# Kernel tuning notes

Hardware: AMD Instinct MI355X
Metric: run time of the kernel (lower is better)

Reference implementation:

```python
import jax, jax.numpy as jnp
import numpy as np

NEG = -1e30  # stand-in for -inf that keeps logaddexp grad-safe


def _ctc_neg_log_likelihood(predictions, labels):
    # predictions: [B, T, C] logits; labels: [B, L] int, -1 = padding.
    # tf.nn.ctc_loss(blank_index=-1) => blank class is C-1.
    B, T, C = predictions.shape
    L = labels.shape[1]
    S = 2 * L + 1
    blank = C - 1

    label_len = jnp.sum((labels != -1).astype(jnp.int32), axis=-1)  # [B]
    labels_c = jnp.where(labels < 0, 0, labels).astype(jnp.int32)

    # Extended label sequence: blank, l1, blank, l2, ..., blank  -> [B, S]
    ext = jnp.full((B, S), blank, dtype=jnp.int32)
    ext = ext.at[:, 1::2].set(labels_c)

    # s-2 transition allowed only at label positions (odd s) with ext[s] != ext[s-2]
    same = jnp.concatenate([jnp.zeros((B, 2), bool), ext[:, 2:] == ext[:, :-2]], axis=1)
    is_label_pos = (jnp.arange(S) % 2 == 1)[None, :]
    allow2 = is_label_pos & ~same  # [B, S]

    # valid extended positions per example: s < 2*label_len + 1
    valid = jnp.arange(S)[None, :] < (2 * label_len + 1)[:, None]  # [B, S]

    log_probs = jax.nn.log_softmax(predictions, axis=-1)  # [B, T, C]
    # emission log-prob for each extended-label slot: [B, T, S]
    lp_ext = jnp.take_along_axis(log_probs, jnp.broadcast_to(ext[:, None, :], (B, T, S)), axis=2)

    has_lab = label_len > 0
    alpha0 = jnp.full((B, S), NEG, dtype=log_probs.dtype)
    alpha0 = alpha0.at[:, 0].set(lp_ext[:, 0, 0])
    alpha0 = alpha0.at[:, 1].set(jnp.where(has_lab, lp_ext[:, 0, 1], NEG))
    alpha0 = jnp.where(valid, alpha0, NEG)

    def step(alpha, lp_t):
        a1 = alpha
        a2 = jnp.pad(alpha, ((0, 0), (1, 0)), constant_values=NEG)[:, :S]
        a3 = jnp.pad(alpha, ((0, 0), (2, 0)), constant_values=NEG)[:, :S]
        a3 = jnp.where(allow2, a3, NEG)
        new = jnp.logaddexp(jnp.logaddexp(a1, a2), a3) + lp_t
        new = jnp.where(valid, new, NEG)
        return new, None

    lp_rest = jnp.moveaxis(lp_ext[:, 1:], 1, 0)  # [T-1, B, S]
    alphaT, _ = jax.lax.scan(step, alpha0, lp_rest)

    idx1 = (2 * label_len)[:, None]              # final blank
    idx2 = jnp.maximum(idx1 - 1, 0)              # final label
    a_end1 = jnp.take_along_axis(alphaT, idx1, axis=1)[:, 0]
    a_end2 = jnp.take_along_axis(alphaT, idx2, axis=1)[:, 0]
    a_end2 = jnp.where(has_lab, a_end2, NEG)
    log_lik = jnp.logaddexp(a_end1, a_end2)
    return -log_lik  # [B]


def setup_inputs() -> dict:
    key = jax.random.key(0)
    k1, k2 = jax.random.split(key)
    B, T, C, L = 1024, 384, 96, 48
    labels = jax.random.randint(k1, (B, L), 0, C - 1).astype(jnp.int64)
    predictions = jax.random.normal(k2, (B, T, C), dtype=jnp.float32)
    return {"labels": labels, "predictions": predictions}


def reference(labels, predictions):
    per_example = _ctc_neg_log_likelihood(predictions, labels)
    return jnp.mean(per_example)
```

## Files before the change

kernel.cpp:

```cpp
#include <hip/hip_runtime.h>

constexpr int Tt = 384;
constexpr int Cc = 96;
constexpr int Ll = 48;
constexpr int Gg = 8;
constexpr int NG = 24;

#define L2E 1.4426950408889634f
#define LN2 0.6931471805599453f
#define LNEG (-3.0e38f)

template <int CTRL, int RM = 0xF>
__device__ __forceinline__ float dppf(float x) {
    return __int_as_float(
        __builtin_amdgcn_update_dpp(0, __float_as_int(x), CTRL, RM, 0xF, true));
}
template <int CTRL>
__device__ __forceinline__ int dppi(int x) {
    return __builtin_amdgcn_update_dpp(0, x, CTRL, 0xF, 0xF, true);
}
__device__ __forceinline__ float bcast63(float x) {
    return __int_as_float(__builtin_amdgcn_readlane(__float_as_int(x), 63));
}
__device__ __forceinline__ float wsum(float x) {
    x += dppf<0x111>(x);
    x += dppf<0x112>(x);
    x += dppf<0x114>(x);
    x += dppf<0x118>(x);
    x += dppf<0x142, 0xA>(x);
    x += dppf<0x143, 0xC>(x);
    return bcast63(x);
}
__device__ __forceinline__ float shup1(float x) { return dppf<0x138>(x); }
__device__ __forceinline__ float shdn1(float x) { return dppf<0x130>(x); }
__device__ __forceinline__ float exp2i(int d) {
    d = d < -126 ? -126 : (d > 126 ? 126 : d);
    return __int_as_float((d + 127) << 23);
}

__global__ __launch_bounds__(512) void ctc_zsum(const float* __restrict__ pred,
                                                float* __restrict__ zs,
                                                float* __restrict__ out) {
    const int b    = blockIdx.x;
    const int lane = threadIdx.x & 63;
    const int wv   = threadIdx.x >> 6;
    const float2* rp2 = (const float2*)(pred + (size_t)b * Tt * Cc);
    __shared__ double part[8];

    if (b == 0 && threadIdx.x == 0) out[0] = 0.0f;

    const int t0 = wv * 48;
    double acc = 0.0;
    float2 qa = (lane < 48) ? rp2[(size_t)t0 * 48 + lane] : make_float2(-1e4f, -1e4f);
    for (int j = 0; j < 48; ++j) {
        float2 qn = qa;
        if (j + 1 < 48)
            qn = (lane < 48) ? rp2[(size_t)(t0 + j + 1) * 48 + lane]
                             : make_float2(-1e4f, -1e4f);
        float ex = __builtin_amdgcn_exp2f(qa.x * L2E);
        float ey = __builtin_amdgcn_exp2f(qa.y * L2E);
        float z  = wsum(ex + ey);
        acc += (double)__log2f(z);
        qa = qn;
    }
    if (lane == 0) part[wv] = acc;
    __syncthreads();
    if (threadIdx.x == 0) {
        double s = 0.0;
#pragma unroll
        for (int w = 0; w < 8; ++w) s += part[w];
        zs[b] = (float)s;
    }
}


template <bool FWD>
__device__ __forceinline__ void dp_load(const float* __restrict__ rp, float* ql,
                                        float* qb, int g, int labv) {
#pragma unroll
    for (int j = 0; j < Gg; ++j) {
        int k = g * Gg + j;
        int t = FWD ? k : (Tt - 1 - k);
        ql[j] = rp[t * Cc + labv];
        qb[j] = rp[t * Cc + 95];
    }
}

template <bool FWD>
__device__ __forceinline__ void dp_group(const float* ql, const float* qb,
                                         float allow2f, float& st_e, float& st_o,
                                         int& ls, float& f, float& a2f) {
    float el[Gg], eb[Gg];
#pragma unroll
    for (int j = 0; j < Gg; ++j) {
        el[j] = __builtin_amdgcn_exp2f(ql[j] * L2E);
        eb[j] = __builtin_amdgcn_exp2f(qb[j] * L2E);
    }
#pragma unroll
    for (int j = 0; j < Gg; ++j) {
        if (FWD) {
            float sh = shup1(st_o);
            float t0 = st_e + st_o;
            float ne = fmaf(f, sh, st_e) * eb[j];
            float no = fmaf(a2f, sh, t0) * el[j];
            st_e = ne; st_o = no;
        } else {
            float en = shdn1(st_e);
            float on = shdn1(st_o);
            float ne = (st_e + st_o) * eb[j];
            float no = fmaf(a2f, on, fmaf(f, en, st_o)) * el[j];
            st_e = ne; st_o = no;
        }
    }
    float m = fmaxf(st_e, st_o);
    bool z  = (m == 0.0f);
    int eb2 = (__float_as_int(m) >> 23) & 0xFF;
    eb2 = eb2 > 253 ? 253 : eb2;
    float r = z ? 1.0f : __int_as_float((254 - eb2) << 23);
    st_e *= r; st_o *= r;
    ls += z ? 0 : (eb2 - 127);
#pragma unroll
    for (int it = 0; it < 8; ++it) {
        int lsn = FWD ? dppi<0x138>(ls) : dppi<0x130>(ls);
        ls = z ? lsn : ls;
    }
    int lsn2 = FWD ? dppi<0x138>(ls) : dppi<0x130>(ls);
    f   = exp2i(lsn2 - ls);
    a2f = allow2f * f;
}

template <bool FWD>
__device__ __forceinline__ void run_half(const float* __restrict__ rp, int labv,
                                         float allow2f, float& st_e, float& st_o,
                                         int& ls, float& f, float& a2f) {
    float qlA[Gg], qbA[Gg], qlB[Gg], qbB[Gg], qlC[Gg], qbC[Gg], qlD[Gg], qbD[Gg];
    dp_load<FWD>(rp, qlA, qbA, 0, labv);
    dp_load<FWD>(rp, qlB, qbB, 1, labv);
    dp_load<FWD>(rp, qlC, qbC, 2, labv);
    dp_load<FWD>(rp, qlD, qbD, 3, labv);
    for (int g4 = 0; g4 < 5; ++g4) {
        int gb = g4 * 4;
        dp_group<FWD>(qlA, qbA, allow2f, st_e, st_o, ls, f, a2f);
        dp_load<FWD>(rp, qlA, qbA, gb + 4, labv);
        dp_group<FWD>(qlB, qbB, allow2f, st_e, st_o, ls, f, a2f);
        dp_load<FWD>(rp, qlB, qbB, gb + 5, labv);
        dp_group<FWD>(qlC, qbC, allow2f, st_e, st_o, ls, f, a2f);
        dp_load<FWD>(rp, qlC, qbC, gb + 6, labv);
        dp_group<FWD>(qlD, qbD, allow2f, st_e, st_o, ls, f, a2f);
        dp_load<FWD>(rp, qlD, qbD, gb + 7, labv);
    }
    dp_group<FWD>(qlA, qbA, allow2f, st_e, st_o, ls, f, a2f);
    dp_group<FWD>(qlB, qbB, allow2f, st_e, st_o, ls, f, a2f);
    dp_group<FWD>(qlC, qbC, allow2f, st_e, st_o, ls, f, a2f);
    dp_group<FWD>(qlD, qbD, allow2f, st_e, st_o, ls, f, a2f);
}

__global__ __launch_bounds__(128) void ctc_dp(const int* __restrict__ labels,
                                              const float* __restrict__ pred,
                                              const float* __restrict__ zs,
                                              float* __restrict__ out,
                                              float invB) {
    const int b    = blockIdx.x;
    const int lane = threadIdx.x & 63;
    const int wv   = threadIdx.x >> 6;
    const float* rp = pred + (size_t)b * Tt * Cc;

    __shared__ float sbe[64], sbo[64];
    __shared__ int   slsb[64];

    float zsb = zs[b];

    int v = (lane < Ll) ? labels[(size_t)b * Ll + lane] : -1;
    int present = (lane < Ll) && (v != -1);
    int labv = (v < 0) ? 0 : v;
    unsigned long long pm = __ballot(present);
    int len = __popcll(pm);
    int lab_p = __shfl(labv, (lane - 1) & 63, 64);
    int lab_n = __shfl(labv, (lane + 1) & 63, 64);

    float st_e, st_o = 0.0f, f = 1.0f, a2f, allow2f;
    int   ls = 0;

    if (wv == 0) {
        allow2f = (lane >= 1 && labv != lab_p) ? 1.0f : 0.0f;
        st_e = (lane == 0) ? 1.0f : 0.0f;
        a2f = allow2f;
        run_half<true>(rp, labv, allow2f, st_e, st_o, ls, f, a2f);
    } else {
        allow2f = (labv != lab_n) ? 1.0f : 0.0f;
        st_e = (lane == len) ? 1.0f : 0.0f;
        a2f = allow2f;
        run_half<false>(rp, labv, allow2f, st_e, st_o, ls, f, a2f);
        sbe[lane]  = st_e;
        sbo[lane]  = st_o;
        slsb[lane] = ls;
    }
    __syncthreads();

    if (wv == 0) {
        float sh  = shup1(st_o);
        int   lsu = dppi<0x138>(ls);
        float fup = exp2i(lsu - ls);
        float Ae = fmaf(fup, sh, st_e);
        float Ao = fmaf(allow2f * fup, sh, st_e + st_o);
        float be = sbe[lane], bo = sbo[lane];
        float base = (float)(ls + slsb[lane]);
        float l1 = (Ae > 0.0f && be > 0.0f) ? __log2f(Ae) + __log2f(be) + base : LNEG;
        float l2 = (Ao > 0.0f && bo > 0.0f) ? __log2f(Ao) + __log2f(bo) + base : LNEG;
        float mm = fmaxf(l1, l2);
#pragma unroll
        for (int off = 32; off >= 1; off >>= 1) mm = fmaxf(mm, __shfl_xor(mm, off, 64));
        float ss = exp2f(l1 - mm) + exp2f(l2 - mm);
#pragma unroll
        for (int off = 32; off >= 1; off >>= 1) ss += __shfl_xor(ss, off, 64);
        if (lane == 0) {
            float ll = (mm + __log2f(ss) - zsb) * LN2;
            atomicAdd(out, -ll * invB);
        }
    }
}

extern "C" void kernel_launch(void* const* d_in, const int* in_sizes, int n_in,
                              void* d_out, int out_size, void* d_ws, size_t ws_size,
                              hipStream_t stream) {
    const int*   labels = (const int*)d_in[0];
    const float* pred   = (const float*)d_in[1];
    float*       out    = (float*)d_out;
    float*       zs     = (float*)d_ws;

    const int B = in_sizes[0] / Ll;

    hipLaunchKernelGGL(ctc_zsum, dim3(B), dim3(512), 0, stream, pred, zs, out);
    hipLaunchKernelGGL(ctc_dp, dim3(B), dim3(128), 0, stream,
                       labels, pred, zs, out, 1.0f / (float)B);
}
```

Baseline: 248.8 us.

## Fuse softmax normalizer and forward-backward DP into one kernel with deterministic mean

The separate log-sum-exp kernel is merged into the DP kernel. Two waves run the forward and backward recursions while six more waves in the same 512-thread block compute the per-row normalizer over 64 timesteps each. The atomic mean is replaced by a per-example NLL buffer and a small reduction kernel. Register prefetch depth drops from four groups to two, presumably to allow launch_bounds(512,8) occupancy. The aim is to remove a launch and the re-read of predictions, and to overlap the normalizer work with the latency-bound DP, at the cost of shallower load prefetching and a hard-coded B=1024 in the mean kernel.

Result: faster. 237.3 us (-4.6%).

```diff
diff --git a/kernel.cpp b/kernel.cpp
--- a/kernel.cpp
+++ b/kernel.cpp
@@ -37,42 +37,6 @@
     d = d < -126 ? -126 : (d > 126 ? 126 : d);
     return __int_as_float((d + 127) << 23);
 }
-
-__global__ __launch_bounds__(512) void ctc_zsum(const float* __restrict__ pred,
-                                                float* __restrict__ zs,
-                                                float* __restrict__ out) {
-    const int b    = blockIdx.x;
-    const int lane = threadIdx.x & 63;
-    const int wv   = threadIdx.x >> 6;
-    const float2* rp2 = (const float2*)(pred + (size_t)b * Tt * Cc);
-    __shared__ double part[8];
-
-    if (b == 0 && threadIdx.x == 0) out[0] = 0.0f;
-
-    const int t0 = wv * 48;
-    double acc = 0.0;
-    float2 qa = (lane < 48) ? rp2[(size_t)t0 * 48 + lane] : make_float2(-1e4f, -1e4f);
-    for (int j = 0; j < 48; ++j) {
-        float2 qn = qa;
-        if (j + 1 < 48)
-            qn = (lane < 48) ? rp2[(size_t)(t0 + j + 1) * 48 + lane]
-                             : make_float2(-1e4f, -1e4f);
-        float ex = __builtin_amdgcn_exp2f(qa.x * L2E);
-        float ey = __builtin_amdgcn_exp2f(qa.y * L2E);
-        float z  = wsum(ex + ey);
-        acc += (double)__log2f(z);
-        qa = qn;
-    }
-    if (lane == 0) part[wv] = acc;
-    __syncthreads();
-    if (threadIdx.x == 0) {
-        double s = 0.0;
-#pragma unroll
-        for (int w = 0; w < 8; ++w) s += part[w];
-        zs[b] = (float)s;
-    }
-}
-
 
 template <bool FWD>
 __device__ __forceinline__ void dp_load(const float* __restrict__ rp, float* ql,
@@ -133,67 +97,73 @@
 __device__ __forceinline__ void run_half(const float* __restrict__ rp, int labv,
                                          float allow2f, float& st_e, float& st_o,
                                          int& ls, float& f, float& a2f) {
-    float qlA[Gg], qbA[Gg], qlB[Gg], qbB[Gg], qlC[Gg], qbC[Gg], qlD[Gg], qbD[Gg];
+    float qlA[Gg], qbA[Gg], qlB[Gg], qbB[Gg];
     dp_load<FWD>(rp, qlA, qbA, 0, labv);
     dp_load<FWD>(rp, qlB, qbB, 1, labv);
-    dp_load<FWD>(rp, qlC, qbC, 2, labv);
-    dp_load<FWD>(rp, qlD, qbD, 3, labv);
-    for (int g4 = 0; g4 < 5; ++g4) {
-        int gb = g4 * 4;
+    for (int g2 = 0; g2 < NG / 2; ++g2) {
+        bool more = (g2 < NG / 2 - 1);
         dp_group<FWD>(qlA, qbA, allow2f, st_e, st_o, ls, f, a2f);
-        dp_load<FWD>(rp, qlA, qbA, gb + 4, labv);
+        if (more) dp_load<FWD>(rp, qlA, qbA, 2 * g2 + 2, labv);
         dp_group<FWD>(qlB, qbB, allow2f, st_e, st_o, ls, f, a2f);
-        dp_load<FWD>(rp, qlB, qbB, gb + 5, labv);
-        dp_group<FWD>(qlC, qbC, allow2f, st_e, st_o, ls, f, a2f);
-        dp_load<FWD>(rp, qlC, qbC, gb + 6, labv);
-        dp_group<FWD>(qlD, qbD, allow2f, st_e, st_o, ls, f, a2f);
-        dp_load<FWD>(rp, qlD, qbD, gb + 7, labv);
-    }
-    dp_group<FWD>(qlA, qbA, allow2f, st_e, st_o, ls, f, a2f);
-    dp_group<FWD>(qlB, qbB, allow2f, st_e, st_o, ls, f, a2f);
-    dp_group<FWD>(qlC, qbC, allow2f, st_e, st_o, ls, f, a2f);
-    dp_group<FWD>(qlD, qbD, allow2f, st_e, st_o, ls, f, a2f);
-}
-
-__global__ __launch_bounds__(128) void ctc_dp(const int* __restrict__ labels,
-                                              const float* __restrict__ pred,
-                                              const float* __restrict__ zs,
-                                              float* __restrict__ out,
-                                              float invB) {
+        if (more) dp_load<FWD>(rp, qlB, qbB, 2 * g2 + 3, labv);
+    }
+}
+
+__global__ __launch_bounds__(512, 8) void ctc_fb(const int* __restrict__ labels,
+                                                 const float* __restrict__ pred,
+                                                 float* __restrict__ nll) {
     const int b    = blockIdx.x;
     const int lane = threadIdx.x & 63;
     const int wv   = threadIdx.x >> 6;
     const float* rp = pred + (size_t)b * Tt * Cc;
 
-    __shared__ float sbe[64], sbo[64];
-    __shared__ int   slsb[64];
-
-    float zsb = zs[b];
-
-    int v = (lane < Ll) ? labels[(size_t)b * Ll + lane] : -1;
-    int present = (lane < Ll) && (v != -1);
-    int labv = (v < 0) ? 0 : v;
-    unsigned long long pm = __ballot(present);
-    int len = __popcll(pm);
-    int lab_p = __shfl(labv, (lane - 1) & 63, 64);
-    int lab_n = __shfl(labv, (lane + 1) & 63, 64);
-
-    float st_e, st_o = 0.0f, f = 1.0f, a2f, allow2f;
+    __shared__ float  sbe[64], sbo[64];
+    __shared__ int    slsb[64];
+    __shared__ double part[6];
+
+    float st_e = 0.0f, st_o = 0.0f, f = 1.0f, a2f = 0.0f, allow2f = 0.0f;
     int   ls = 0;
-
-    if (wv == 0) {
-        allow2f = (lane >= 1 && labv != lab_p) ? 1.0f : 0.0f;
-        st_e = (lane == 0) ? 1.0f : 0.0f;
-        a2f = allow2f;
-        run_half<true>(rp, labv, allow2f, st_e, st_o, ls, f, a2f);
+    int   labv = 0, len = 0;
+
+    if (wv < 2) {
+        int v = (lane < Ll) ? labels[(size_t)b * Ll + lane] : -1;
+        int present = (lane < Ll) && (v != -1);
+        labv = (v < 0) ? 0 : v;
+        unsigned long long pm = __ballot(present);
+        len = __popcll(pm);
+        int lab_p = __shfl(labv, (lane - 1) & 63, 64);
+        int lab_n = __shfl(labv, (lane + 1) & 63, 64);
+        if (wv == 0) {
+            allow2f = (lane >= 1 && labv != lab_p) ? 1.0f : 0.0f;
+            st_e = (lane == 0) ? 1.0f : 0.0f;
+            a2f = allow2f;
+            run_half<true>(rp, labv, allow2f, st_e, st_o, ls, f, a2f);
+        } else {
+            allow2f = (labv != lab_n) ? 1.0f : 0.0f;
+            st_e = (lane == len) ? 1.0f : 0.0f;
+            a2f = allow2f;
+            run_half<false>(rp, labv, allow2f, st_e, st_o, ls, f, a2f);
+            sbe[lane]  = st_e;
+            sbo[lane]  = st_o;
+            slsb[lane] = ls;
+        }
     } else {
-        allow2f = (labv != lab_n) ? 1.0f : 0.0f;
-        st_e = (lane == len) ? 1.0f : 0.0f;
-        a2f = allow2f;
-        run_half<false>(rp, labv, allow2f, st_e, st_o, ls, f, a2f);
-        sbe[lane]  = st_e;
-        sbo[lane]  = st_o;
-        slsb[lane] = ls;
+        const float2* rp2 = (const float2*)rp;
+        const int t0 = (wv - 2) * 64;
+        double acc = 0.0;
+        float2 qa = (lane < 48) ? rp2[(size_t)t0 * 48 + lane] : make_float2(-1e4f, -1e4f);
+        for (int j = 0; j < 64; ++j) {
+            float2 qn = qa;
+            if (j + 1 < 64)
+                qn = (lane < 48) ? rp2[(size_t)(t0 + j + 1) * 48 + lane]
+                                 : make_float2(-1e4f, -1e4f);
+            float ex = __builtin_amdgcn_exp2f(qa.x * L2E);
+            float ey = __builtin_amdgcn_exp2f(qa.y * L2E);
+            float z  = wsum(ex + ey);
+            acc += (double)__log2f(z);
+            qa = qn;
+        }
+        if (lane == 0) part[wv - 2] = acc;
     }
     __syncthreads();
 
@@ -214,10 +184,29 @@
 #pragma unroll
         for (int off = 32; off >= 1; off >>= 1) ss += __shfl_xor(ss, off, 64);
         if (lane == 0) {
-            float ll = (mm + __log2f(ss) - zsb) * LN2;
-            atomicAdd(out, -ll * invB);
-        }
-    }
+            double zt = 0.0;
+#pragma unroll
+            for (int w = 0; w < 6; ++w) zt += part[w];
+            float ll = (mm + __log2f(ss) - (float)zt) * LN2;
+            nll[b] = -ll;
+        }
+    }
+}
+
+__global__ __launch_bounds__(256) void ctc_mean(const float* __restrict__ nll,
+                                                float* __restrict__ out, float invB) {
+    __shared__ double part[256];
+    double s = 0.0;
+#pragma unroll
+    for (int i = 0; i < 4; ++i) s += (double)nll[threadIdx.x + 256 * i];
+    part[threadIdx.x] = s;
+    __syncthreads();
+#pragma unroll
+    for (int w = 128; w >= 1; w >>= 1) {
+        if (threadIdx.x < w) part[threadIdx.x] += part[threadIdx.x + w];
+        __syncthreads();
+    }
+    if (threadIdx.x == 0) out[0] = (float)(part[0] * (double)invB);
 }
 
 extern "C" void kernel_launch(void* const* d_in, const int* in_sizes, int n_in,
@@ -226,11 +215,10 @@
     const int*   labels = (const int*)d_in[0];
     const float* pred   = (const float*)d_in[1];
     float*       out    = (float*)d_out;
-    float*       zs     = (float*)d_ws;
+    float*       nll    = (float*)d_ws;
 
     const int B = in_sizes[0] / Ll;
 
-    hipLaunchKernelGGL(ctc_zsum, dim3(B), dim3(512), 0, stream, pred, zs, out);
-    hipLaunchKernelGGL(ctc_dp, dim3(B), dim3(128), 0, stream,
-                       labels, pred, zs, out, 1.0f / (float)B);
-}
+    hipLaunchKernelGGL(ctc_fb, dim3(B), dim3(512), 0, stream, labels, pred, nll);
+    hipLaunchKernelGGL(ctc_mean, dim3(1), dim3(256), 0, stream, nll, out, 1.0f / (float)B);
+}
```
